# Kernel tuning notes

Hardware: AMD Instinct MI355X
Metric: run time of the kernel (lower is better)

Reference implementation:

```python
import jax, jax.numpy as jnp
import numpy as np


def _lstm_scan(xproj, Wh, h0, c0):
    """xproj: [T,B,4H] precomputed input projections (order f,i,o,c). Returns hidden seq [T,B,H]."""
    H = h0.shape[-1]
    def step(carry, xp):
        h, c = carry
        g = xp + h @ Wh.T                      # [B,4H]
        f = jax.nn.sigmoid(g[:, :H])
        i = jax.nn.sigmoid(g[:, H:2 * H])
        o = jax.nn.sigmoid(g[:, 2 * H:3 * H])
        ch = jnp.tanh(g[:, 3 * H:])
        c = f * c + i * ch
        h = o * jnp.tanh(c)
        return (h, c), h
    _, hs = jax.lax.scan(step, (h0, c0), xproj)
    return hs


def setup_inputs() -> dict:
    key = jax.random.key(0)
    ks = jax.random.split(key, 13)
    B, T, I, H, O = 32, 512, 256, 512, 128
    s_g = 1.0 / np.sqrt(I + H)
    s_o = 1.0 / np.sqrt(2 * H)
    return {
        "x": jax.random.normal(ks[0], (B, T, I), jnp.float32),
        "Wf_w": jax.random.normal(ks[1], (H, I + H), jnp.float32) * s_g,
        "Wf_b": jax.random.normal(ks[2], (H,), jnp.float32) * s_g,
        "Wi_w": jax.random.normal(ks[3], (H, I + H), jnp.float32) * s_g,
        "Wi_b": jax.random.normal(ks[4], (H,), jnp.float32) * s_g,
        "Wo_w": jax.random.normal(ks[5], (H, I + H), jnp.float32) * s_g,
        "Wo_b": jax.random.normal(ks[6], (H,), jnp.float32) * s_g,
        "Wc_w": jax.random.normal(ks[7], (H, I + H), jnp.float32) * s_g,
        "Wc_b": jax.random.normal(ks[8], (H,), jnp.float32) * s_g,
        "out_w": jax.random.normal(ks[9], (O, 2 * H), jnp.float32) * s_o,
        "out_b": jax.random.normal(ks[10], (O,), jnp.float32) * s_o,
        "bh0": jax.random.normal(ks[11], (1, H), jnp.float32),
        "bc0": jax.random.normal(ks[12], (1, H), jnp.float32),
    }


def reference(x, Wf_w, Wf_b, Wi_w, Wi_b, Wo_w, Wo_b, Wc_w, Wc_b, out_w, out_b, bh0, bc0):
    B, T, I = x.shape
    H = Wf_b.shape[0]
    # Concatenated gate weights (f,i,o,c) split into input / recurrent parts.
    W = jnp.concatenate([Wf_w, Wi_w, Wo_w, Wc_w], axis=0)    # [4H, I+H]
    b = jnp.concatenate([Wf_b, Wi_b, Wo_b, Wc_b], axis=0)    # [4H]
    Wx, Wh = W[:, :I], W[:, I:]
    xproj = jnp.einsum('bti,gi->tbg', x, Wx) + b             # [T,B,4H]
    # Forward direction: zero init. Backward: learned init, same weights.
    z = jnp.zeros((B, H), x.dtype)
    hf = _lstm_scan(xproj, Wh, z, z)                          # [T,B,H]
    hb = _lstm_scan(xproj[::-1], Wh,
                    jnp.broadcast_to(bh0, (B, H)),
                    jnp.broadcast_to(bc0, (B, H)))[::-1]      # [T,B,H]
    outs = jnp.concatenate([hf, hb], axis=-1).transpose(1, 0, 2)  # [B,T,2H]
    return outs @ out_w.T + out_b                             # [B,T,O]
```

## Files before the change

kernel.cpp:

```cpp
#include <hip/hip_runtime.h>
#include <hip/hip_bf16.h>

#define Bb 32
#define Tt 512
#define Ii 256
#define Hh 512
#define Oo 128
#define NG 32

using bf16x8 = __attribute__((ext_vector_type(8))) __bf16;
using f32x4  = __attribute__((ext_vector_type(4))) float;

__device__ __forceinline__ bf16x8 f32x8_to_bf16(const float* p) {
    const float4 u = *reinterpret_cast<const float4*>(p);
    const float4 v = *reinterpret_cast<const float4*>(p + 4);
    bf16x8 r;
    r[0] = (__bf16)u.x; r[1] = (__bf16)u.y; r[2] = (__bf16)u.z; r[3] = (__bf16)u.w;
    r[4] = (__bf16)v.x; r[5] = (__bf16)v.y; r[6] = (__bf16)v.z; r[7] = (__bf16)v.w;
    return r;
}

__global__ void k_setup(const float* __restrict__ bh0,
                        __bf16* __restrict__ hinit, int* __restrict__ flags) {
    const int tid = blockIdx.x * 256 + threadIdx.x;
    if (tid < 64) flags[tid] = 0;
    if (tid < Bb * Hh) {
        hinit[tid] = (__bf16)0.f;
        hinit[Bb * Hh + tid] = (__bf16)bh0[tid & (Hh - 1)];
    }
}

__global__ __launch_bounds__(256) void k_xproj(
    const float* __restrict__ x,
    const float* __restrict__ Wf, const float* __restrict__ bf_,
    const float* __restrict__ Wi, const float* __restrict__ bi_,
    const float* __restrict__ Wo, const float* __restrict__ bo_,
    const float* __restrict__ Wc, const float* __restrict__ bc_,
    __bf16* __restrict__ xproj)
{
    const int wgM = blockIdx.x;
    const int wgN = blockIdx.y;
    const int tid = threadIdx.x;
    const int wave = tid >> 6, lane = tid & 63;
    const int mw = wave >> 1, nw = wave & 1;
    const int l15 = lane & 15, lhi = lane >> 4;

    const int gamma = wgN >> 2;
    const float* W    = (gamma == 0) ? Wf : (gamma == 1) ? Wi : (gamma == 2) ? Wo : Wc;
    const float* bptr = (gamma == 0) ? bf_ : (gamma == 1) ? bi_ : (gamma == 2) ? bo_ : bc_;

    f32x4 acc[2][4];
#pragma unroll
    for (int m = 0; m < 2; m++)
#pragma unroll
        for (int n = 0; n < 4; n++) acc[m][n] = f32x4{0.f, 0.f, 0.f, 0.f};

    const int rowbase = wgM * 64 + mw * 32;
    const int colbase = wgN * 128 + nw * 64;

#pragma unroll
    for (int kk = 0; kk < 8; ++kk) {
        const int k0 = kk * 32 + lhi * 8;
        bf16x8 a[2], b[4];
#pragma unroll
        for (int m = 0; m < 2; m++) {
            const int r = rowbase + m * 16 + l15;
            a[m] = f32x8_to_bf16(x + (long)r * Ii + k0);
        }
#pragma unroll
        for (int n = 0; n < 4; n++) {
            const int g = colbase + n * 16 + l15;
            b[n] = f32x8_to_bf16(W + (long)(g & 511) * 768 + k0);
        }
#pragma unroll
        for (int m = 0; m < 2; m++)
#pragma unroll
            for (int n = 0; n < 4; n++)
                acc[m][n] = __builtin_amdgcn_mfma_f32_16x16x32_bf16(a[m], b[n], acc[m][n], 0, 0, 0);
    }

#pragma unroll
    for (int m = 0; m < 2; m++)
#pragma unroll
        for (int n = 0; n < 4; n++) {
            const int g = colbase + n * 16 + l15;
            const float bias = bptr[g & 511];
#pragma unroll
            for (int r = 0; r < 4; r++) {
                const int R = rowbase + m * 16 + lhi * 4 + r;
                const int t = R & (Tt - 1), bb = R >> 9;
                xproj[((long)t * Bb + bb) * 2048 + g] = (__bf16)(acc[m][n][r] + bias);
            }
        }
}

__global__ __launch_bounds__(256) void k_rec(
    const float* __restrict__ Wf, const float* __restrict__ Wi,
    const float* __restrict__ Wo, const float* __restrict__ Wc,
    const float* __restrict__ bc0,
    const __bf16* __restrict__ xproj,
    __bf16* __restrict__ hs,
    const __bf16* __restrict__ hinit,
    int* flags)
{
    const int dir  = blockIdx.x >> 5;
    const int gsel = blockIdx.x & 31;
    const int tid  = threadIdx.x;
    const int wave = tid >> 6;
    const int lane = tid & 63;
    const int l15  = lane & 15, lhi = lane >> 4;

    __shared__ __bf16 hlds[32 * 512];
    __shared__ float  gbuf[32][65];

    const float* Wp = (wave == 0) ? Wf : (wave == 1) ? Wi : (wave == 2) ? Wo : Wc;
    const float* wrow = Wp + (long)(gsel * 16 + l15) * 768 + Ii;
    bf16x8 bfrag[16];
#pragma unroll
    for (int kk = 0; kk < 16; ++kk) bfrag[kk] = f32x8_to_bf16(wrow + kk * 32 + lhi * 8);

    const int b_ew = tid & 31;
    const int hc0  = (tid >> 5) * 2;
    float c0s = (dir == 0) ? 0.f : bc0[gsel * 16 + hc0];
    float c1s = (dir == 0) ? 0.f : bc0[gsel * 16 + hc0 + 1];

    int* flagd = flags + dir * 32;
    __bf16* hsd = hs + (long)dir * Tt * Bb * Hh;

    const int ck = tid & 63;
    const int r0 = tid >> 6;
    char* lbase = reinterpret_cast<char*>(hlds);

    for (int s = 0; s < Tt; ++s) {
        const int t = (dir == 0) ? s : (Tt - 1 - s);

        const __bf16* xp = xproj + ((long)t * Bb + b_ew) * 2048;
        float x0[4], x1[4];
#pragma unroll
        for (int g = 0; g < 4; ++g) {
            const unsigned int xv =
                *reinterpret_cast<const unsigned int*>(xp + g * 512 + gsel * 16 + hc0);
            x0[g] = __builtin_bit_cast(float, xv << 16);
            x1[g] = __builtin_bit_cast(float, xv & 0xffff0000u);
        }

        if (s > 0 && wave == 0) {
            const int src = lane & 31;
            for (int p = 0; p < 4096; ++p) {
                const int f = __hip_atomic_load(flagd + src, __ATOMIC_RELAXED,
                                                __HIP_MEMORY_SCOPE_AGENT);
                if (__all(f >= s)) break;
                __builtin_amdgcn_s_sleep(2);
            }
        }
        __syncthreads();

        const __bf16* hp = (s == 0) ? (hinit + (long)dir * Bb * Hh)
                                    : (hsd + (long)((dir == 0) ? (t - 1) : (t + 1)) * Bb * Hh);
        const char* gb = reinterpret_cast<const char*>(hp) + r0 * 1024 + ck * 16;
        f32x4 v0, v1, v2, v3, v4, v5, v6, v7;
#define LDC(i, dst) asm volatile("global_load_dwordx4 %0, %1, off sc0 sc1" \
                                 : "=&v"(dst) : "v"(gb + (i) * 4096) : "memory")
        LDC(0, v0); LDC(1, v1); LDC(2, v2); LDC(3, v3);
        LDC(4, v4); LDC(5, v5); LDC(6, v6); LDC(7, v7);
#undef LDC
        asm volatile("s_waitcnt vmcnt(0)" ::: "memory");
        __builtin_amdgcn_sched_barrier(0);
#define STC(i, src) { const int r = r0 + 4 * (i); \
        *reinterpret_cast<f32x4*>(lbase + r * 1024 + ((ck * 16) ^ ((r & 7) << 4))) = src; }
        STC(0, v0); STC(1, v1); STC(2, v2); STC(3, v3);
        STC(4, v4); STC(5, v5); STC(6, v6); STC(7, v7);
#undef STC
        __syncthreads();

        f32x4 acc0 = f32x4{0.f, 0.f, 0.f, 0.f};
        f32x4 acc1 = f32x4{0.f, 0.f, 0.f, 0.f};
#pragma unroll
        for (int kk = 0; kk < 16; ++kk) {
            const int kb = kk * 64 + lhi * 16;
            const int rr0 = l15, rr1 = 16 + l15;
            bf16x8 a0 = *reinterpret_cast<const bf16x8*>(
                lbase + rr0 * 1024 + (kb ^ ((rr0 & 7) << 4)));
            bf16x8 a1 = *reinterpret_cast<const bf16x8*>(
                lbase + rr1 * 1024 + (kb ^ ((rr1 & 7) << 4)));
            acc0 = __builtin_amdgcn_mfma_f32_16x16x32_bf16(a0, bfrag[kk], acc0, 0, 0, 0);
            acc1 = __builtin_amdgcn_mfma_f32_16x16x32_bf16(a1, bfrag[kk], acc1, 0, 0, 0);
        }
#pragma unroll
        for (int r = 0; r < 4; ++r) {
            gbuf[lhi * 4 + r][wave * 16 + l15]      = acc0[r];
            gbuf[16 + lhi * 4 + r][wave * 16 + l15] = acc1[r];
        }
        __syncthreads();

        float h0, h1;
        {
            const float gf = x0[0] + gbuf[b_ew][hc0];
            const float gi = x0[1] + gbuf[b_ew][16 + hc0];
            const float go = x0[2] + gbuf[b_ew][32 + hc0];
            const float gc = x0[3] + gbuf[b_ew][48 + hc0];
            const float f  = 1.f / (1.f + __expf(-gf));
            const float ii = 1.f / (1.f + __expf(-gi));
            const float oo = 1.f / (1.f + __expf(-go));
            c0s = f * c0s + ii * tanhf(gc);
            h0 = oo * tanhf(c0s);
        }
        {
            const float gf = x1[0] + gbuf[b_ew][hc0 + 1];
            const float gi = x1[1] + gbuf[b_ew][16 + hc0 + 1];
            const float go = x1[2] + gbuf[b_ew][32 + hc0 + 1];
            const float gc = x1[3] + gbuf[b_ew][48 + hc0 + 1];
            const float f  = 1.f / (1.f + __expf(-gf));
            const float ii = 1.f / (1.f + __expf(-gi));
            const float oo = 1.f / (1.f + __expf(-go));
            c1s = f * c1s + ii * tanhf(gc);
            h1 = oo * tanhf(c1s);
        }
        const __bf16 b0 = (__bf16)h0, b1 = (__bf16)h1;
        const unsigned int packed =
            ((unsigned int)__builtin_bit_cast(unsigned short, b1) << 16) |
            (unsigned int)__builtin_bit_cast(unsigned short, b0);
        char* dst = reinterpret_cast<char*>(hsd + ((long)t * Bb + b_ew) * Hh + gsel * 16 + hc0);
        asm volatile("global_store_dword %0, %1, off sc0 sc1"
                     :: "v"(dst), "v"(packed) : "memory");
        asm volatile("s_waitcnt vmcnt(0)" ::: "memory");
        __syncthreads();
        if (tid == 0)
            __hip_atomic_store(flagd + gsel, s + 1, __ATOMIC_RELAXED,
                               __HIP_MEMORY_SCOPE_AGENT);
    }
}

__global__ __launch_bounds__(256) void k_out(
    const __bf16* __restrict__ hs,
    const float* __restrict__ out_w,
    const float* __restrict__ out_b,
    float* __restrict__ out)
{
    const int wgM = blockIdx.x;
    const int tid = threadIdx.x;
    const int wave = tid >> 6, lane = tid & 63;
    const int mw = wave >> 1, nw = wave & 1;
    const int l15 = lane & 15, lhi = lane >> 4;

    f32x4 acc[2][4];
#pragma unroll
    for (int m = 0; m < 2; m++)
#pragma unroll
        for (int n = 0; n < 4; n++) acc[m][n] = f32x4{0.f, 0.f, 0.f, 0.f};

    const int rowbase = wgM * 64 + mw * 32;
    const int colbase = nw * 64;

#pragma unroll 4
    for (int kk = 0; kk < 32; ++kk) {
        const int k0 = kk * 32 + lhi * 8;
        const int d = k0 >> 9, hk = k0 & 511;
        bf16x8 a[2], b[4];
#pragma unroll
        for (int m = 0; m < 2; m++) {
            const int R = rowbase + m * 16 + l15;
            a[m] = *reinterpret_cast<const bf16x8*>(hs + ((long)d * 16384 + R) * 512 + hk);
        }
#pragma unroll
        for (int n = 0; n < 4; n++) {
            const int o = colbase + n * 16 + l15;
            b[n] = f32x8_to_bf16(out_w + (long)o * 1024 + k0);
        }
#pragma unroll
        for (int m = 0; m < 2; m++)
#pragma unroll
            for (int n = 0; n < 4; n++)
                acc[m][n] = __builtin_amdgcn_mfma_f32_16x16x32_bf16(a[m], b[n], acc[m][n], 0, 0, 0);
    }

#pragma unroll
    for (int m = 0; m < 2; m++)
#pragma unroll
        for (int n = 0; n < 4; n++) {
            const int o = colbase + n * 16 + l15;
            const float bias = out_b[o];
#pragma unroll
            for (int r = 0; r < 4; r++) {
                const int R = rowbase + m * 16 + lhi * 4 + r;
                const int tt = R >> 5, bb = R & 31;
                out[((long)bb * Tt + tt) * Oo + o] = acc[m][n][r] + bias;
            }
        }
}

extern "C" void kernel_launch(void* const* d_in, const int* in_sizes, int n_in,
                              void* d_out, int out_size, void* d_ws, size_t ws_size,
                              hipStream_t stream) {
    (void)in_sizes; (void)n_in; (void)out_size; (void)ws_size;
    const float* x    = (const float*)d_in[0];
    const float* Wf_w = (const float*)d_in[1];
    const float* Wf_b = (const float*)d_in[2];
    const float* Wi_w = (const float*)d_in[3];
    const float* Wi_b = (const float*)d_in[4];
    const float* Wo_w = (const float*)d_in[5];
    const float* Wo_b = (const float*)d_in[6];
    const float* Wc_w = (const float*)d_in[7];
    const float* Wc_b = (const float*)d_in[8];
    const float* out_w = (const float*)d_in[9];
    const float* out_b = (const float*)d_in[10];
    const float* bh0  = (const float*)d_in[11];
    const float* bc0  = (const float*)d_in[12];

    char* ws = (char*)d_ws;
    __bf16* xproj = (__bf16*)(ws);
    __bf16* hs    = (__bf16*)(ws + 67108864);
    __bf16* hinit = (__bf16*)(ws + 100663296);
    int*    flags = (int*)   (ws + 100728832);

    k_setup<<<64, 256, 0, stream>>>(bh0, hinit, flags);
    dim3 g1(256, 16);
    k_xproj<<<g1, 256, 0, stream>>>(x, Wf_w, Wf_b, Wi_w, Wi_b, Wo_w, Wo_b, Wc_w, Wc_b, xproj);
    k_rec<<<2 * NG, 256, 0, stream>>>(Wf_w, Wi_w, Wo_w, Wc_w, bc0, xproj, hs, hinit, flags);
    k_out<<<256, 256, 0, stream>>>(hs, out_w, out_b, (float*)d_out);
}
```

Measured before the change: 2.263 ms.

## Repartition recurrent kernel into 8 wider 512-thread blocks per direction with per-wave flags

The recurrent LSTM kernel now runs on 8 workgroups per direction of 512 threads each, instead of 32 workgroups of 256. Each wave holds 32 gate rows of recurrent weights in registers, and each thread updates 4 hidden units. Fewer blocks means fewer participants in the per-step global flag barrier, and per-wave flags replace the trailing __syncthreads. It also swaps tanhf for an exp-based tanh and widens the h store to dwordx2. The risks are higher register pressure from doubling the weight fragments, and more MFMA work serialized per CU on each step.

```diff
diff --git a/kernel.cpp b/kernel.cpp
--- a/kernel.cpp
+++ b/kernel.cpp
@@ -6,7 +6,7 @@
 #define Ii 256
 #define Hh 512
 #define Oo 128
-#define NG 32
+#define NG 8
 
 using bf16x8 = __attribute__((ext_vector_type(8))) __bf16;
 using f32x4  = __attribute__((ext_vector_type(4))) float;
@@ -20,10 +20,23 @@
     return r;
 }
 
+__device__ __forceinline__ float sigm(float x) { return 1.f / (1.f + __expf(-x)); }
+__device__ __forceinline__ float tanh_fast(float x) {
+    const float e = __expf(2.f * x);
+    return 1.f - 2.f / (e + 1.f);
+}
+__device__ __forceinline__ unsigned short bfbits(float x) {
+    return __builtin_bit_cast(unsigned short, (__bf16)x);
+}
+__device__ __forceinline__ float bsel(uint2 u, int j) {
+    const unsigned w = (j & 2) ? u.y : u.x;
+    return __builtin_bit_cast(float, (j & 1) ? (w & 0xffff0000u) : (w << 16));
+}
+
 __global__ void k_setup(const float* __restrict__ bh0,
                         __bf16* __restrict__ hinit, int* __restrict__ flags) {
     const int tid = blockIdx.x * 256 + threadIdx.x;
-    if (tid < 64) flags[tid] = 0;
+    if (tid < 128) flags[tid] = 0;
     if (tid < Bb * Hh) {
         hinit[tid] = (__bf16)0.f;
         hinit[Bb * Hh + tid] = (__bf16)bh0[tid & (Hh - 1)];
@@ -94,7 +107,7 @@
         }
 }
 
-__global__ __launch_bounds__(256) void k_rec(
+__global__ __launch_bounds__(512, 2) void k_rec(
     const float* __restrict__ Wf, const float* __restrict__ Wi,
     const float* __restrict__ Wo, const float* __restrict__ Wc,
     const float* __restrict__ bc0,
@@ -103,130 +116,134 @@
     const __bf16* __restrict__ hinit,
     int* flags)
 {
-    const int dir  = blockIdx.x >> 5;
-    const int gsel = blockIdx.x & 31;
+    const int dir  = blockIdx.x >> 3;
+    const int gsel = blockIdx.x & 7;
     const int tid  = threadIdx.x;
     const int wave = tid >> 6;
     const int lane = tid & 63;
     const int l15  = lane & 15, lhi = lane >> 4;
-
-    __shared__ __bf16 hlds[32 * 512];
-    __shared__ float  gbuf[32][65];
-
-    const float* Wp = (wave == 0) ? Wf : (wave == 1) ? Wi : (wave == 2) ? Wo : Wc;
-    const float* wrow = Wp + (long)(gsel * 16 + l15) * 768 + Ii;
-    bf16x8 bfrag[16];
-#pragma unroll
-    for (int kk = 0; kk < 16; ++kk) bfrag[kk] = f32x8_to_bf16(wrow + kk * 32 + lhi * 8);
+    const int g    = wave >> 1;
+    const int ch   = wave & 1;
+
+    __shared__ __bf16 hlds[Bb * Hh];
+    __shared__ float  gbuf[Bb * 256];
+
+    const float* Wp = (g == 0) ? Wf : (g == 1) ? Wi : (g == 2) ? Wo : Wc;
+    bf16x8 bfrag[2][16];
+#pragma unroll
+    for (int n = 0; n < 2; n++)
+#pragma unroll
+        for (int kk = 0; kk < 16; kk++) {
+            const int row = gsel * 64 + ch * 32 + n * 16 + l15;
+            bfrag[n][kk] = f32x8_to_bf16(Wp + (long)row * 768 + Ii + kk * 32 + lhi * 8);
+        }
 
     const int b_ew = tid & 31;
-    const int hc0  = (tid >> 5) * 2;
-    float c0s = (dir == 0) ? 0.f : bc0[gsel * 16 + hc0];
-    float c1s = (dir == 0) ? 0.f : bc0[gsel * 16 + hc0 + 1];
-
-    int* flagd = flags + dir * 32;
+    const int c4   = (tid >> 5) * 4;
+    float cs[4];
+#pragma unroll
+    for (int j = 0; j < 4; j++)
+        cs[j] = (dir == 0) ? 0.f : bc0[gsel * 64 + c4 + j];
+
+    int* flagd = flags + dir * 64;
     __bf16* hsd = hs + (long)dir * Tt * Bb * Hh;
-
-    const int ck = tid & 63;
-    const int r0 = tid >> 6;
     char* lbase = reinterpret_cast<char*>(hlds);
+    char* gbase = reinterpret_cast<char*>(gbuf);
 
     for (int s = 0; s < Tt; ++s) {
         const int t = (dir == 0) ? s : (Tt - 1 - s);
 
-        const __bf16* xp = xproj + ((long)t * Bb + b_ew) * 2048;
-        float x0[4], x1[4];
-#pragma unroll
-        for (int g = 0; g < 4; ++g) {
-            const unsigned int xv =
-                *reinterpret_cast<const unsigned int*>(xp + g * 512 + gsel * 16 + hc0);
-            x0[g] = __builtin_bit_cast(float, xv << 16);
-            x1[g] = __builtin_bit_cast(float, xv & 0xffff0000u);
-        }
+        const __bf16* xp = xproj + ((long)t * Bb + b_ew) * 2048 + gsel * 64 + c4;
+        uint2 xr[4];
+#pragma unroll
+        for (int g2 = 0; g2 < 4; g2++)
+            xr[g2] = *reinterpret_cast<const uint2*>(xp + g2 * 512);
 
         if (s > 0 && wave == 0) {
-            const int src = lane & 31;
             for (int p = 0; p < 4096; ++p) {
-                const int f = __hip_atomic_load(flagd + src, __ATOMIC_RELAXED,
+                const int f = __hip_atomic_load(flagd + lane, __ATOMIC_RELAXED,
                                                 __HIP_MEMORY_SCOPE_AGENT);
                 if (__all(f >= s)) break;
-                __builtin_amdgcn_s_sleep(2);
+                __builtin_amdgcn_s_sleep(1);
             }
         }
         __syncthreads();
 
         const __bf16* hp = (s == 0) ? (hinit + (long)dir * Bb * Hh)
                                     : (hsd + (long)((dir == 0) ? (t - 1) : (t + 1)) * Bb * Hh);
-        const char* gb = reinterpret_cast<const char*>(hp) + r0 * 1024 + ck * 16;
-        f32x4 v0, v1, v2, v3, v4, v5, v6, v7;
-#define LDC(i, dst) asm volatile("global_load_dwordx4 %0, %1, off sc0 sc1" \
-                                 : "=&v"(dst) : "v"(gb + (i) * 4096) : "memory")
-        LDC(0, v0); LDC(1, v1); LDC(2, v2); LDC(3, v3);
-        LDC(4, v4); LDC(5, v5); LDC(6, v6); LDC(7, v7);
-#undef LDC
+        const char* gb0 = reinterpret_cast<const char*>(hp) + wave * 1024 + lane * 16;
+        f32x4 v0, v1, v2, v3;
+        asm volatile("global_load_dwordx4 %0, %1, off sc0 sc1" : "=&v"(v0) : "v"(gb0) : "memory");
+        asm volatile("global_load_dwordx4 %0, %1, off sc0 sc1" : "=&v"(v1) : "v"(gb0 + 8192) : "memory");
+        asm volatile("global_load_dwordx4 %0, %1, off sc0 sc1" : "=&v"(v2) : "v"(gb0 + 16384) : "memory");
+        asm volatile("global_load_dwordx4 %0, %1, off sc0 sc1" : "=&v"(v3) : "v"(gb0 + 24576) : "memory");
         asm volatile("s_waitcnt vmcnt(0)" ::: "memory");
         __builtin_amdgcn_sched_barrier(0);
-#define STC(i, src) { const int r = r0 + 4 * (i); \
-        *reinterpret_cast<f32x4*>(lbase + r * 1024 + ((ck * 16) ^ ((r & 7) << 4))) = src; }
-        STC(0, v0); STC(1, v1); STC(2, v2); STC(3, v3);
-        STC(4, v4); STC(5, v5); STC(6, v6); STC(7, v7);
-#undef STC
+        {
+            const int r0 = wave, r1 = wave + 8, r2 = wave + 16, r3 = wave + 24;
+            *reinterpret_cast<f32x4*>(lbase + r0 * 1024 + ((lane * 16) ^ ((r0 & 7) << 4))) = v0;
+            *reinterpret_cast<f32x4*>(lbase + r1 * 1024 + ((lane * 16) ^ ((r1 & 7) << 4))) = v1;
+            *reinterpret_cast<f32x4*>(lbase + r2 * 1024 + ((lane * 16) ^ ((r2 & 7) << 4))) = v2;
+            *reinterpret_cast<f32x4*>(lbase + r3 * 1024 + ((lane * 16) ^ ((r3 & 7) << 4))) = v3;
+        }
         __syncthreads();
 
-        f32x4 acc0 = f32x4{0.f, 0.f, 0.f, 0.f};
-        f32x4 acc1 = f32x4{0.f, 0.f, 0.f, 0.f};
+        f32x4 acc[2][2];
+#pragma unroll
+        for (int m = 0; m < 2; m++)
+#pragma unroll
+            for (int n = 0; n < 2; n++) acc[m][n] = f32x4{0.f, 0.f, 0.f, 0.f};
 #pragma unroll
         for (int kk = 0; kk < 16; ++kk) {
             const int kb = kk * 64 + lhi * 16;
-            const int rr0 = l15, rr1 = 16 + l15;
+            const int r0 = l15, r1 = 16 + l15;
             bf16x8 a0 = *reinterpret_cast<const bf16x8*>(
-                lbase + rr0 * 1024 + (kb ^ ((rr0 & 7) << 4)));
+                lbase + r0 * 1024 + (kb ^ ((r0 & 7) << 4)));
             bf16x8 a1 = *reinterpret_cast<const bf16x8*>(
-                lbase + rr1 * 1024 + (kb ^ ((rr1 & 7) << 4)));
-            acc0 = __builtin_amdgcn_mfma_f32_16x16x32_bf16(a0, bfrag[kk], acc0, 0, 0, 0);
-            acc1 = __builtin_amdgcn_mfma_f32_16x16x32_bf16(a1, bfrag[kk], acc1, 0, 0, 0);
-        }
-#pragma unroll
-        for (int r = 0; r < 4; ++r) {
-            gbuf[lhi * 4 + r][wave * 16 + l15]      = acc0[r];
-            gbuf[16 + lhi * 4 + r][wave * 16 + l15] = acc1[r];
-        }
+                lbase + r1 * 1024 + (kb ^ ((r1 & 7) << 4)));
+            acc[0][0] = __builtin_amdgcn_mfma_f32_16x16x32_bf16(a0, bfrag[0][kk], acc[0][0], 0, 0, 0);
+            acc[0][1] = __builtin_amdgcn_mfma_f32_16x16x32_bf16(a0, bfrag[1][kk], acc[0][1], 0, 0, 0);
+            acc[1][0] = __builtin_amdgcn_mfma_f32_16x16x32_bf16(a1, bfrag[0][kk], acc[1][0], 0, 0, 0);
+            acc[1][1] = __builtin_amdgcn_mfma_f32_16x16x32_bf16(a1, bfrag[1][kk], acc[1][1], 0, 0, 0);
+        }
+#pragma unroll
+        for (int m = 0; m < 2; m++)
+#pragma unroll
+            for (int n = 0; n < 2; n++)
+#pragma unroll
+                for (int r = 0; r < 4; r++) {
+                    const int row = m * 16 + lhi * 4 + r;
+                    const int col = g * 64 + ch * 32 + n * 16 + l15;
+                    *reinterpret_cast<float*>(
+                        gbase + row * 1024 + ((col * 4) ^ ((row & 7) << 4))) = acc[m][n][r];
+                }
         __syncthreads();
 
-        float h0, h1;
-        {
-            const float gf = x0[0] + gbuf[b_ew][hc0];
-            const float gi = x0[1] + gbuf[b_ew][16 + hc0];
-            const float go = x0[2] + gbuf[b_ew][32 + hc0];
-            const float gc = x0[3] + gbuf[b_ew][48 + hc0];
-            const float f  = 1.f / (1.f + __expf(-gf));
-            const float ii = 1.f / (1.f + __expf(-gi));
-            const float oo = 1.f / (1.f + __expf(-go));
-            c0s = f * c0s + ii * tanhf(gc);
-            h0 = oo * tanhf(c0s);
-        }
-        {
-            const float gf = x1[0] + gbuf[b_ew][hc0 + 1];
-            const float gi = x1[1] + gbuf[b_ew][16 + hc0 + 1];
-            const float go = x1[2] + gbuf[b_ew][32 + hc0 + 1];
-            const float gc = x1[3] + gbuf[b_ew][48 + hc0 + 1];
-            const float f  = 1.f / (1.f + __expf(-gf));
-            const float ii = 1.f / (1.f + __expf(-gi));
-            const float oo = 1.f / (1.f + __expf(-go));
-            c1s = f * c1s + ii * tanhf(gc);
-            h1 = oo * tanhf(c1s);
-        }
-        const __bf16 b0 = (__bf16)h0, b1 = (__bf16)h1;
-        const unsigned int packed =
-            ((unsigned int)__builtin_bit_cast(unsigned short, b1) << 16) |
-            (unsigned int)__builtin_bit_cast(unsigned short, b0);
-        char* dst = reinterpret_cast<char*>(hsd + ((long)t * Bb + b_ew) * Hh + gsel * 16 + hc0);
-        asm volatile("global_store_dword %0, %1, off sc0 sc1"
-                     :: "v"(dst), "v"(packed) : "memory");
+        f32x4 G[4];
+#pragma unroll
+        for (int g2 = 0; g2 < 4; g2++)
+            G[g2] = *reinterpret_cast<const f32x4*>(
+                gbase + b_ew * 1024 + (((g2 * 64 + c4) * 4) ^ ((b_ew & 7) << 4)));
+        float hv[4];
+#pragma unroll
+        for (int j = 0; j < 4; j++) {
+            const float gf = bsel(xr[0], j) + G[0][j];
+            const float gi = bsel(xr[1], j) + G[1][j];
+            const float go = bsel(xr[2], j) + G[2][j];
+            const float gc = bsel(xr[3], j) + G[3][j];
+            const float ff = sigm(gf), ii2 = sigm(gi), oo2 = sigm(go);
+            cs[j] = ff * cs[j] + ii2 * tanh_fast(gc);
+            hv[j] = oo2 * tanh_fast(cs[j]);
+        }
+        const unsigned long long pk =
+            ((unsigned long long)(((unsigned)bfbits(hv[3]) << 16) | bfbits(hv[2])) << 32) |
+            (((unsigned)bfbits(hv[1]) << 16) | bfbits(hv[0]));
+        char* dst = reinterpret_cast<char*>(hsd + ((long)t * Bb + b_ew) * Hh + gsel * 64 + c4);
+        asm volatile("global_store_dwordx2 %0, %1, off sc0 sc1"
+                     :: "v"(dst), "v"(pk) : "memory");
         asm volatile("s_waitcnt vmcnt(0)" ::: "memory");
-        __syncthreads();
-        if (tid == 0)
-            __hip_atomic_store(flagd + gsel, s + 1, __ATOMIC_RELAXED,
+        if (lane == 0)
+            __hip_atomic_store(flagd + gsel * 8 + wave, s + 1, __ATOMIC_RELAXED,
                                __HIP_MEMORY_SCOPE_AGENT);
     }
 }
@@ -316,6 +333,6 @@
     k_setup<<<64, 256, 0, stream>>>(bh0, hinit, flags);
     dim3 g1(256, 16);
     k_xproj<<<g1, 256, 0, stream>>>(x, Wf_w, Wf_b, Wi_w, Wi_b, Wo_w, Wo_b, Wc_w, Wc_b, xproj);
-    k_rec<<<2 * NG, 256, 0, stream>>>(Wf_w, Wi_w, Wo_w, Wc_w, bc0, xproj, hs, hinit, flags);
+    k_rec<<<2 * NG, 512, 0, stream>>>(Wf_w, Wi_w, Wo_w, Wc_w, bc0, xproj, hs, hinit, flags);
     k_out<<<256, 256, 0, stream>>>(hs, out_w, out_b, (float*)d_out);
 }
```

After: 3.598 ms. 59.0% more time.
